# Performance work log

Measured on AMD Instinct MI355X. Metric: run time of the kernel, lower is better.

Reference implementation:

```python
import jax, jax.numpy as jnp
import numpy as np

B, N, D = 4, 2048, 1024
H, A, Lv = 8, 128, 128   # heads, attention_dim (qk), linear_dim (v)
NUM_BLOCKS = 4
QKV_W = (2 * Lv + 2 * A) * H  # 4096
NEG = -1e9


def setup_inputs() -> dict:
    key = jax.random.key(0)
    ks = jax.random.split(key, 10)
    past_lengths = jax.random.randint(ks[0], (B,), 0, N)
    past_ids = jax.random.randint(ks[1], (B, N), 0, 10000)
    past_embeddings = jax.random.normal(ks[2], (B, N, D), dtype=jnp.float32)
    # per-block parameters, stacked on leading block axis (xavier-ish scale)
    qkv_w = jax.random.normal(ks[3], (NUM_BLOCKS, D, QKV_W), dtype=jnp.float32) * (1.0 / np.sqrt(D))
    qkv_b = jnp.zeros((NUM_BLOCKS, QKV_W), dtype=jnp.float32)
    out_w = jax.random.normal(ks[4], (NUM_BLOCKS, Lv * H, D), dtype=jnp.float32) * (1.0 / np.sqrt(Lv * H))
    out_b = jnp.zeros((NUM_BLOCKS, D), dtype=jnp.float32)
    ln_g = jnp.ones((NUM_BLOCKS, D), dtype=jnp.float32)
    ln_b = jnp.zeros((NUM_BLOCKS, D), dtype=jnp.float32)
    return {"past_lengths": past_lengths, "past_ids": past_ids,
            "past_embeddings": past_embeddings, "qkv_w": qkv_w, "qkv_b": qkv_b,
            "out_w": out_w, "out_b": out_b, "ln_g": ln_g, "ln_b": ln_b}


def _layer_norm(x, g, b, eps=1e-5):
    mu = jnp.mean(x, axis=-1, keepdims=True)
    var = jnp.mean(jnp.square(x - mu), axis=-1, keepdims=True)
    return (x - mu) * jax.lax.rsqrt(var + eps) * g + b


def _block(x, mask, qw, qb, ow, ob, g, b):
    xn = _layer_norm(x, g, b)
    qkv = (xn @ qw + qb).reshape(B, N, H, 2 * Lv + 2 * A)
    q = qkv[..., :A]              # [B,N,H,A]
    k = qkv[..., A:2 * A]         # [B,N,H,A]
    v = qkv[..., 2 * A:2 * A + Lv]  # [B,N,H,Lv]
    scores = jnp.einsum('bnha,bmha->bhnm', q, k) / np.sqrt(A)
    # original: masked_fill(-inf) -> silu -> /N -> softmax; we mask after the
    # silu transform with a large-negative logit so masked weights are ~0
    logits = jnp.where(mask[:, None, :, :], jax.nn.silu(scores) / N, NEG)
    w = jax.nn.softmax(logits, axis=-1)
    attn = jnp.einsum('bhnm,bmhl->bnhl', w, v).reshape(B, N, H * Lv)
    return x + attn @ ow + ob


def reference(past_lengths, past_ids, past_embeddings, qkv_w, qkv_b, out_w, out_b, ln_g, ln_b):
    valid = past_ids != 0                                   # [B,N]
    causal = jnp.triu(jnp.ones((N, N), dtype=bool), k=1)     # faithful to buffer (triu, diag=1)
    mask = causal[None] & valid[:, None, :] & valid[:, :, None]  # [B,N,N]
    x = past_embeddings
    for i in range(NUM_BLOCKS):
        x = _block(x, mask, qkv_w[i], qkv_b[i], out_w[i], out_b[i], ln_g[i], ln_b[i])
    return x
```

## Files before the change

### kernel.cpp

```cpp
#include <hip/hip_runtime.h>

typedef __bf16 bf16_t;
typedef __bf16 bf16x8 __attribute__((ext_vector_type(8)));
typedef __bf16 bf16x4 __attribute__((ext_vector_type(4)));
typedef float f32x4 __attribute__((ext_vector_type(4)));

#define B_ 4
#define N_ 2048
#define D_ 1024
#define H_ 8
#define NB_ 4
#define M_ (B_*N_)
#define QN_ 3072
#define QKN_ 2048

__device__ __forceinline__ void async_copy16(const void* gsrc, void* ldst) {
    __builtin_amdgcn_global_load_lds(
        (const __attribute__((address_space(1))) void*)gsrc,
        (__attribute__((address_space(3))) void*)ldst, 16, 0, 0);
}

static constexpr size_t WT_OFF  = 0;
static constexpr size_t WT_SZ   = (size_t)NB_*QN_*D_*2;
static constexpr size_t OWT_OFF = WT_OFF + WT_SZ;
static constexpr size_t OWT_SZ  = (size_t)NB_*D_*D_*2;
static constexpr size_t XN_OFF  = OWT_OFF + OWT_SZ;
static constexpr size_t XN_SZ   = (size_t)M_*D_*2;
static constexpr size_t QK_OFF  = XN_OFF + XN_SZ;
static constexpr size_t QK_SZ   = (size_t)M_*QKN_*2;
static constexpr size_t VT_OFF  = QK_OFF + QK_SZ;
static constexpr size_t VT_SZ   = (size_t)32*128*N_*2;
static constexpr size_t ATT_OFF = VT_OFF + VT_SZ;
static constexpr size_t ATT_SZ  = (size_t)M_*D_*2;
static constexpr size_t QBR_OFF = ATT_OFF + ATT_SZ;
static constexpr size_t QBR_SZ  = (size_t)NB_*QN_*4;
static constexpr size_t VS_OFF  = QBR_OFF + QBR_SZ;

__global__ __launch_bounds__(256) void repack_qkvw(const float* __restrict__ qw, bf16_t* __restrict__ wt)
{
    __shared__ float tile[64][65];
    const int nb = blockIdx.z;
    const int j0 = blockIdx.x * 64, d0 = blockIdx.y * 64;
    const int tx = threadIdx.x, ty = threadIdx.y;
    const float* src = qw + (size_t)nb * D_ * 4096;
    const int jj = j0 + tx;
    const int sel = jj >> 10, rr = jj & 1023, hh = rr >> 7, aa = rr & 127;
    const int orig = hh * 512 + sel * 128 + aa;
#pragma unroll
    for (int it = 0; it < 16; ++it) {
        int dr = it * 4 + ty;
        tile[dr][tx] = src[(size_t)(d0 + dr) * 4096 + orig];
    }
    __syncthreads();
    bf16_t* dst = wt + (size_t)nb * QN_ * D_;
#pragma unroll
    for (int it = 0; it < 16; ++it) {
        int jr = it * 4 + ty;
        dst[(size_t)(j0 + jr) * D_ + d0 + tx] = (bf16_t)tile[tx][jr];
    }
}

__global__ __launch_bounds__(256) void repack_outw(const float* __restrict__ ow, bf16_t* __restrict__ owt)
{
    __shared__ float tile[64][65];
    const int nb = blockIdx.z;
    const int j0 = blockIdx.x * 64, d0 = blockIdx.y * 64;
    const int tx = threadIdx.x, ty = threadIdx.y;
    const float* src = ow + (size_t)nb * D_ * D_;
#pragma unroll
    for (int it = 0; it < 16; ++it) {
        int dr = it * 4 + ty;
        tile[dr][tx] = src[(size_t)(d0 + dr) * D_ + j0 + tx];
    }
    __syncthreads();
    bf16_t* dst = owt + (size_t)nb * D_ * D_;
#pragma unroll
    for (int it = 0; it < 16; ++it) {
        int jr = it * 4 + ty;
        dst[(size_t)(j0 + jr) * D_ + d0 + tx] = (bf16_t)tile[tx][jr];
    }
}

__global__ __launch_bounds__(256) void repack_qb(const float* __restrict__ qb, float* __restrict__ qbr)
{
    int idx = blockIdx.x * 256 + threadIdx.x;
    int nb = idx / QN_, jj = idx % QN_;
    int sel = jj >> 10, rr = jj & 1023, hh = rr >> 7, aa = rr & 127;
    qbr[idx] = qb[nb * 4096 + hh * 512 + sel * 128 + aa];
}

__global__ __launch_bounds__(256) void ln_kernel(const float* __restrict__ x, const float* __restrict__ g,
                                                 const float* __restrict__ bb, bf16_t* __restrict__ xn)
{
    const int row = blockIdx.x, tid = threadIdx.x;
    const float4 v = ((const float4*)(x + (size_t)row * D_))[tid];
    float s = v.x + v.y + v.z + v.w;
    float q = v.x * v.x + v.y * v.y + v.z * v.z + v.w * v.w;
#pragma unroll
    for (int d = 32; d >= 1; d >>= 1) { s += __shfl_xor(s, d); q += __shfl_xor(q, d); }
    __shared__ float ls[4], lq[4];
    if ((tid & 63) == 0) { ls[tid >> 6] = s; lq[tid >> 6] = q; }
    __syncthreads();
    s = ls[0] + ls[1] + ls[2] + ls[3];
    q = lq[0] + lq[1] + lq[2] + lq[3];
    const float mean = s * (1.f / 1024.f);
    const float var  = q * (1.f / 1024.f) - mean * mean;
    const float inv  = rsqrtf(var + 1e-5f);
    const float4 gg = ((const float4*)g)[tid];
    const float4 bv = ((const float4*)bb)[tid];
    bf16x4 o;
    o[0] = (bf16_t)((v.x - mean) * inv * gg.x + bv.x);
    o[1] = (bf16_t)((v.y - mean) * inv * gg.y + bv.y);
    o[2] = (bf16_t)((v.z - mean) * inv * gg.z + bv.z);
    o[3] = (bf16_t)((v.w - mean) * inv * gg.w + bv.w);
    *(bf16x4*)(xn + (size_t)row * D_ + tid * 4) = o;
}

template<bool RESID>
__global__ __launch_bounds__(512, 2) void gemm256(const bf16_t* __restrict__ Am, const bf16_t* __restrict__ Bt,
                                                  const float* __restrict__ bias, float* __restrict__ resid_out,
                                                  bf16_t* __restrict__ outH, bf16_t* __restrict__ vtOut,
                                                  int Kn, int Nn, int vSplit)
{
    __shared__ bf16_t As[4 * 256 * 32];
    __shared__ bf16_t Bs[4 * 128 * 32];
    const int tid = threadIdx.x;
    const int lane = tid & 63, wave = tid >> 6;
    const int wr = wave >> 2, wc = wave & 3;
    const int quad = lane >> 4, l15 = lane & 15;
    const int swz = quad ^ ((l15 >> 1) & 3);
    const int slane8 = ((lane & 3) ^ ((lane >> 3) & 3)) * 8;
    const int lrow = lane >> 2;
    const int m0 = blockIdx.y * 256, n0 = blockIdx.x * 128;

    const int chA0 = wave * 2, chA1 = chA0 + 1;
    const bf16_t* gA0 = Am + (size_t)(m0 + chA0 * 16 + lrow) * Kn + slane8;
    const bf16_t* gA1 = Am + (size_t)(m0 + chA1 * 16 + lrow) * Kn + slane8;
    const bf16_t* gB  = Bt + (size_t)(n0 + wave * 16 + lrow) * Kn + slane8;
    bf16_t* const dA0 = &As[chA0 * 512];
    bf16_t* const dA1 = &As[chA1 * 512];
    bf16_t* const dB  = &Bs[wave * 512];

    auto STAGE = [&](int slot) {
        async_copy16(gA0, dA0 + slot * 8192);
        async_copy16(gA1, dA1 + slot * 8192);
        async_copy16(gB,  dB  + slot * 4096);
        gA0 += 32; gA1 += 32; gB += 32;
    };

    f32x4 acc[8][2] = {};
    const int NT = Kn >> 5;

    STAGE(0); STAGE(1); STAGE(2);
    asm volatile("s_waitcnt vmcnt(6)" ::: "memory");
    __builtin_amdgcn_s_barrier();

    const int aoff = (wr * 128 + l15) * 32 + swz * 8;
    const int boff = (wc * 32  + l15) * 32 + swz * 8;

    for (int t = 0; t < NT; ++t) {
        const int ring = t & 3;
        const bf16_t* ra = &As[ring * 8192 + aoff];
        const bf16_t* rb = &Bs[ring * 4096 + boff];
        bf16x8 af[8], bfv[2];
#pragma unroll
        for (int i = 0; i < 8; ++i) af[i] = *(const bf16x8*)(ra + i * 512);
#pragma unroll
        for (int j = 0; j < 2; ++j) bfv[j] = *(const bf16x8*)(rb + j * 512);
        if (t + 3 < NT) STAGE((t + 3) & 3);
        __builtin_amdgcn_s_barrier();
        asm volatile("s_waitcnt lgkmcnt(0)" ::: "memory");
        __builtin_amdgcn_s_setprio(1);
#pragma unroll
        for (int i = 0; i < 8; ++i)
#pragma unroll
            for (int j = 0; j < 2; ++j)
                acc[i][j] = __builtin_amdgcn_mfma_f32_16x16x32_bf16(af[i], bfv[j], acc[i][j], 0, 0, 0);
        __builtin_amdgcn_s_setprio(0);
        if (t + 3 < NT)      asm volatile("s_waitcnt vmcnt(6)" ::: "memory");
        else if (t + 2 < NT) asm volatile("s_waitcnt vmcnt(3)" ::: "memory");
        else if (t + 1 < NT) asm volatile("s_waitcnt vmcnt(0)" ::: "memory");
        __builtin_amdgcn_s_barrier();
    }

    if (!RESID && n0 >= vSplit) {
#pragma unroll
        for (int i = 0; i < 8; ++i) {
            const int rowg = m0 + wr * 128 + i * 16 + quad * 4;
            const int bb2 = rowg >> 11, mloc = rowg & 2047;
#pragma unroll
            for (int j = 0; j < 2; ++j) {
                const int colg = n0 + wc * 32 + j * 16 + l15;
                const int hh = (colg - 2048) >> 7, ll = (colg - 2048) & 127;
                const float bv = bias[colg];
                bf16x4 sv;
#pragma unroll
                for (int r = 0; r < 4; ++r) sv[r] = (bf16_t)(acc[i][j][r] + bv);
                *(bf16x4*)(vtOut + ((size_t)(bb2 * 8 + hh) * 128 + ll) * (size_t)N_ + mloc) = sv;
            }
        }
        return;
    }
#pragma unroll
    for (int i = 0; i < 8; ++i) {
#pragma unroll
        for (int j = 0; j < 2; ++j) {
            const int colg = n0 + wc * 32 + j * 16 + l15;
            const float bv = bias[colg];
#pragma unroll
            for (int r = 0; r < 4; ++r) {
                const int rowg = m0 + wr * 128 + i * 16 + quad * 4 + r;
                const size_t off = (size_t)rowg * Nn + colg;
                const float v = acc[i][j][r] + bv;
                if (RESID) resid_out[off] += v;
                else       outH[off] = (bf16_t)v;
            }
        }
    }
}

__global__ __launch_bounds__(256) void vsum_kernel(const bf16_t* __restrict__ vt, float* __restrict__ vs)
{
    const int gid = blockIdx.x * 4 + (threadIdx.x >> 6);
    const int lane = threadIdx.x & 63;
    const bf16_t* p = vt + (size_t)gid * N_ + lane * 8;
    float s = 0.f;
#pragma unroll
    for (int c = 0; c < 4; ++c) {
        bf16x8 v = *(const bf16x8*)(p + c * 512);
#pragma unroll
        for (int u = 0; u < 8; ++u) s += (float)v[u];
    }
#pragma unroll
    for (int d = 32; d >= 1; d >>= 1) s += __shfl_xor(s, d);
    if (lane == 0) vs[gid] = s;
}

template<bool CAUSAL>
__device__ __forceinline__ void attn_tile(
    int m0, int n0, int b, int h,
    const bf16_t* __restrict__ qk, const bf16_t* __restrict__ vtb,
    const int* __restrict__ past_ids,
    bf16_t* Ks, float* vmf, bf16_t* Ps,
    const bf16x8* qf, bf16x8 onesf, float vnf,
    f32x4* oacc, f32x4& dacc)
{
    const int tid = threadIdx.x, lane = tid & 63, wave = tid >> 6;
    const int quad = lane >> 4, l15 = lane & 15;
    const int swz = quad ^ ((l15 >> 1) & 3);
    const int slane8 = ((lane & 3) ^ ((lane >> 3) & 3)) * 8;
    const int lrow = lane >> 2;
    const size_t baseq = (size_t)b * N_ * QKN_;
    const float scaleA = 0.08838834764831845f;
    const float invN = 1.f / 2048.f;

    __syncthreads();
#pragma unroll
    for (int s = 0; s < 8; ++s) {
        const int kkc = s & 3, rg = (s >> 2) + wave * 2;
        async_copy16(qk + baseq + (size_t)(m0 + rg * 16 + lrow) * QKN_ + 1024 + h * 128 + kkc * 32 + slane8,
                     &Ks[kkc * 4096 + rg * 512 + lane * 8]);
    }
    if (tid < 128) vmf[tid] = past_ids[b * N_ + m0 + tid] != 0 ? 1.f : 0.f;
    __syncthreads();

    f32x4 sacc[8] = {};
#pragma unroll
    for (int kk = 0; kk < 4; ++kk) {
#pragma unroll
        for (int j = 0; j < 8; ++j) {
            bf16x8 kf = *(const bf16x8*)&Ks[kk * 4096 + (j * 16 + l15) * 32 + swz * 8];
            sacc[j] = __builtin_amdgcn_mfma_f32_16x16x32_bf16(kf, qf[kk], sacc[j], 0, 0, 0);
        }
    }
    __syncthreads();

#pragma unroll
    for (int s = 0; s < 8; ++s) {
        const int kkc = s & 3, rg = (s >> 2) + wave * 2;
        async_copy16(vtb + (size_t)(rg * 16 + lrow) * N_ + m0 + kkc * 32 + slane8,
                     &Ks[kkc * 4096 + rg * 512 + lane * 8]);
    }

    const int dbase = CAUSAL ? (m0 - n0 - wave * 16 - l15 + quad * 4) : 0;
#pragma unroll
    for (int j = 0; j < 8; ++j) {
        f32x4 mmv = *(const f32x4*)&vmf[j * 16 + quad * 4];
        bf16x4 pv;
#pragma unroll
        for (int r = 0; r < 4; ++r) {
            const float sv = sacc[j][r] * scaleA;
            const float xc = fminf(fmaxf(sv, -4.f), 4.f);
            float sig = __builtin_fmaf(xc, 0.25f, 0.5f);
            sig = __builtin_fmaf(-(xc * 0.03125f), fabsf(xc), sig);
            float e = __builtin_fmaf(sv * sig, invN, 1.f);
            e *= mmv[r] * vnf;
            if (CAUSAL) e = (dbase + j * 16 + r > 0) ? e : 0.f;
            pv[r] = (bf16_t)e;
        }
        const int cc = (j & 1) * 2 + (quad >> 1);
        const int cp = cc ^ ((l15 >> 1) & 3);
        *(bf16x4*)&Ps[wave * 2048 + (j >> 1) * 512 + l15 * 32 + cp * 8 + (quad & 1) * 4] = pv;
    }
    __syncthreads();

#pragma unroll
    for (int kk = 0; kk < 4; ++kk) {
        bf16x8 pf = *(const bf16x8*)&Ps[wave * 2048 + kk * 512 + l15 * 32 + swz * 8];
        dacc = __builtin_amdgcn_mfma_f32_16x16x32_bf16(pf, onesf, dacc, 0, 0, 0);
#pragma unroll
        for (int j = 0; j < 8; ++j) {
            bf16x8 vf = *(const bf16x8*)&Ks[kk * 4096 + (j * 16 + l15) * 32 + swz * 8];
            oacc[j] = __builtin_amdgcn_mfma_f32_16x16x32_bf16(pf, vf, oacc[j], 0, 0, 0);
        }
    }
}

__global__ __launch_bounds__(256, 3) void attn_kernel(const bf16_t* __restrict__ qk, const bf16_t* __restrict__ vt,
                                                      const int* __restrict__ past_ids, const float* __restrict__ vsum,
                                                      bf16_t* __restrict__ att)
{
    __shared__ bf16_t Ks[4 * 128 * 32];
    __shared__ bf16_t Ps[4 * 2048];
    __shared__ float vmf[128];

    const int bx = blockIdx.x;
    const int bh = bx & 31, t = bx >> 5;
    const int b = bh >> 3, h = bh & 7;
    const int n0 = t << 6;
    const int tid = threadIdx.x, lane = tid & 63, wave = tid >> 6;
    const int quad = lane >> 4, l15 = lane & 15;
    const bf16_t* vtb = vt + (size_t)bh * 128 * N_;
    const float invN = 1.f / 2048.f;

    bf16x8 qf[4];
    {
        const bf16_t* gq = qk + (size_t)b * N_ * QKN_ + (size_t)(n0 + wave * 16 + l15) * QKN_ + h * 128 + quad * 8;
#pragma unroll
        for (int kk = 0; kk < 4; ++kk) qf[kk] = *(const bf16x8*)(gq + kk * 32);
    }
    const float vnf = past_ids[b * N_ + n0 + wave * 16 + l15] != 0 ? 1.f : 0.f;
    bf16x8 onesf;
#pragma unroll
    for (int i = 0; i < 8; ++i) onesf[i] = (bf16_t)1.f;

    f32x4 oacc[8] = {};
    f32x4 dacc = {};

    const int mt0 = t >> 1;
    attn_tile<true>(mt0 << 7, n0, b, h, qk, vtb, past_ids, Ks, vmf, Ps, qf, onesf, vnf, oacc, dacc);
    for (int mt = mt0 + 1; mt < 16; ++mt)
        attn_tile<false>(mt << 7, n0, b, h, qk, vtb, past_ids, Ks, vmf, Ps, qf, onesf, vnf, oacc, dacc);

    float vsr[8];
#pragma unroll
    for (int j = 0; j < 8; ++j) vsr[j] = vsum[bh * 128 + j * 16 + l15];
#pragma unroll
    for (int r = 0; r < 4; ++r) {
        const float dn = dacc[r];
        const bool uni = !(dn > 0.f);
        const float rc = uni ? 0.f : __builtin_amdgcn_rcpf(dn);
        const int gn = n0 + wave * 16 + quad * 4 + r;
#pragma unroll
        for (int j = 0; j < 8; ++j) {
            const int col = j * 16 + l15;
            const float ov = uni ? (vsr[j] * invN) : (oacc[j][r] * rc);
            att[(size_t)(b * N_ + gn) * 1024 + h * 128 + col] = (bf16_t)ov;
        }
    }
}

extern "C" void kernel_launch(void* const* d_in, const int* in_sizes, int n_in,
                              void* d_out, int out_size, void* d_ws, size_t ws_size,
                              hipStream_t stream) {
    (void)in_sizes; (void)n_in; (void)out_size; (void)ws_size;
    const int*   past_ids = (const int*)d_in[1];
    const float* past_emb = (const float*)d_in[2];
    const float* qkv_w    = (const float*)d_in[3];
    const float* qkv_b    = (const float*)d_in[4];
    const float* out_w    = (const float*)d_in[5];
    const float* out_b    = (const float*)d_in[6];
    const float* ln_g     = (const float*)d_in[7];
    const float* ln_b     = (const float*)d_in[8];

    float* x = (float*)d_out;
    char* ws = (char*)d_ws;
    bf16_t* WT  = (bf16_t*)(ws + WT_OFF);
    bf16_t* OWT = (bf16_t*)(ws + OWT_OFF);
    bf16_t* XN  = (bf16_t*)(ws + XN_OFF);
    bf16_t* QK  = (bf16_t*)(ws + QK_OFF);
    bf16_t* VT  = (bf16_t*)(ws + VT_OFF);
    bf16_t* ATT = (bf16_t*)(ws + ATT_OFF);
    float*  QBR = (float*)(ws + QBR_OFF);
    float*  VS  = (float*)(ws + VS_OFF);

    hipMemcpyAsync(x, past_emb, (size_t)M_ * D_ * sizeof(float), hipMemcpyDeviceToDevice, stream);
    repack_qkvw<<<dim3(48, 16, NB_), dim3(64, 4), 0, stream>>>(qkv_w, WT);
    repack_outw<<<dim3(16, 16, NB_), dim3(64, 4), 0, stream>>>(out_w, OWT);
    repack_qb<<<48, 256, 0, stream>>>(qkv_b, QBR);

    for (int layer = 0; layer < NB_; ++layer) {
        ln_kernel<<<M_, 256, 0, stream>>>(x, ln_g + layer * D_, ln_b + layer * D_, XN);
        gemm256<false><<<dim3(QN_ / 128, M_ / 256), 512, 0, stream>>>(
            XN, WT + (size_t)layer * QN_ * D_, QBR + layer * QN_, nullptr, QK, VT, D_, QKN_, 2048);
        vsum_kernel<<<1024, 256, 0, stream>>>(VT, VS);
        attn_kernel<<<1024, 256, 0, stream>>>(QK, VT, past_ids, VS, ATT);
        gemm256<true><<<dim3(D_ / 128, M_ / 256), 512, 0, stream>>>(
            ATT, OWT + (size_t)layer * D_ * D_, out_b + layer * D_, x, nullptr, nullptr, D_, D_, 1 << 30);
    }
}
```

Measured before the change: 929.5 us.

## Restructure attention to 128-query tiles with register P and prefetched K

Each attention block now handles 128 queries (two 16-row groups per wave), so every K/V tile load is reused across twice as many queries. The P matrix is kept in registers instead of a shared-memory round trip, which needs a matching row permutation of the V-transpose output in the QKV GEMM epilogue. The validity mask is built once per block as ballot bitmasks, and the next K tile is loaded during the PV MFMAs. The grid is halved with a paired causal schedule to balance work, and occupancy drops to 2 blocks per unit because of higher register and LDS use.

```diff
diff --git a/kernel.cpp b/kernel.cpp
--- a/kernel.cpp
+++ b/kernel.cpp
@@ -188,6 +188,7 @@
         for (int i = 0; i < 8; ++i) {
             const int rowg = m0 + wr * 128 + i * 16 + quad * 4;
             const int bb2 = rowg >> 11, mloc = rowg & 2047;
+            const int mperm = (mloc & ~31) | (((mloc >> 2) & 3) << 3) | (((mloc >> 4) & 1) << 2);
 #pragma unroll
             for (int j = 0; j < 2; ++j) {
                 const int colg = n0 + wc * 32 + j * 16 + l15;
@@ -196,7 +197,7 @@
                 bf16x4 sv;
 #pragma unroll
                 for (int r = 0; r < 4; ++r) sv[r] = (bf16_t)(acc[i][j][r] + bv);
-                *(bf16x4*)(vtOut + ((size_t)(bb2 * 8 + hh) * 128 + ll) * (size_t)N_ + mloc) = sv;
+                *(bf16x4*)(vtOut + ((size_t)(bb2 * 8 + hh) * 128 + ll) * (size_t)N_ + mperm) = sv;
             }
         }
         return;
@@ -238,134 +239,175 @@
 
 template<bool CAUSAL>
 __device__ __forceinline__ void attn_tile(
-    int m0, int n0, int b, int h,
+    int m0, int m0n, int n0, int b, int h,
     const bf16_t* __restrict__ qk, const bf16_t* __restrict__ vtb,
-    const int* __restrict__ past_ids,
-    bf16_t* Ks, float* vmf, bf16_t* Ps,
-    const bf16x8* qf, bf16x8 onesf, float vnf,
-    f32x4* oacc, f32x4& dacc)
+    bf16_t* Ks, bf16_t* Vs, const unsigned int* mb,
+    const bf16x8 (&qf)[2][4], bf16x8 onesf, float vnf0, float vnf1,
+    f32x4 (&oacc)[2][8], f32x4 (&dacc)[2])
 {
     const int tid = threadIdx.x, lane = tid & 63, wave = tid >> 6;
     const int quad = lane >> 4, l15 = lane & 15;
     const int swz = quad ^ ((l15 >> 1) & 3);
     const int slane8 = ((lane & 3) ^ ((lane >> 3) & 3)) * 8;
     const int lrow = lane >> 2;
-    const size_t baseq = (size_t)b * N_ * QKN_;
     const float scaleA = 0.08838834764831845f;
     const float invN = 1.f / 2048.f;
-
-    __syncthreads();
-#pragma unroll
-    for (int s = 0; s < 8; ++s) {
-        const int kkc = s & 3, rg = (s >> 2) + wave * 2;
-        async_copy16(qk + baseq + (size_t)(m0 + rg * 16 + lrow) * QKN_ + 1024 + h * 128 + kkc * 32 + slane8,
-                     &Ks[kkc * 4096 + rg * 512 + lane * 8]);
-    }
-    if (tid < 128) vmf[tid] = past_ids[b * N_ + m0 + tid] != 0 ? 1.f : 0.f;
-    __syncthreads();
-
-    f32x4 sacc[8] = {};
-#pragma unroll
-    for (int kk = 0; kk < 4; ++kk) {
-#pragma unroll
-        for (int j = 0; j < 8; ++j) {
-            bf16x8 kf = *(const bf16x8*)&Ks[kk * 4096 + (j * 16 + l15) * 32 + swz * 8];
-            sacc[j] = __builtin_amdgcn_mfma_f32_16x16x32_bf16(kf, qf[kk], sacc[j], 0, 0, 0);
-        }
-    }
-    __syncthreads();
 
 #pragma unroll
     for (int s = 0; s < 8; ++s) {
         const int kkc = s & 3, rg = (s >> 2) + wave * 2;
         async_copy16(vtb + (size_t)(rg * 16 + lrow) * N_ + m0 + kkc * 32 + slane8,
-                     &Ks[kkc * 4096 + rg * 512 + lane * 8]);
-    }
-
-    const int dbase = CAUSAL ? (m0 - n0 - wave * 16 - l15 + quad * 4) : 0;
-#pragma unroll
-    for (int j = 0; j < 8; ++j) {
-        f32x4 mmv = *(const f32x4*)&vmf[j * 16 + quad * 4];
-        bf16x4 pv;
-#pragma unroll
-        for (int r = 0; r < 4; ++r) {
-            const float sv = sacc[j][r] * scaleA;
-            const float xc = fminf(fmaxf(sv, -4.f), 4.f);
-            float sig = __builtin_fmaf(xc, 0.25f, 0.5f);
-            sig = __builtin_fmaf(-(xc * 0.03125f), fabsf(xc), sig);
-            float e = __builtin_fmaf(sv * sig, invN, 1.f);
-            e *= mmv[r] * vnf;
-            if (CAUSAL) e = (dbase + j * 16 + r > 0) ? e : 0.f;
-            pv[r] = (bf16_t)e;
-        }
-        const int cc = (j & 1) * 2 + (quad >> 1);
-        const int cp = cc ^ ((l15 >> 1) & 3);
-        *(bf16x4*)&Ps[wave * 2048 + (j >> 1) * 512 + l15 * 32 + cp * 8 + (quad & 1) * 4] = pv;
-    }
-    __syncthreads();
-
+                     &Vs[kkc * 4096 + rg * 512 + lane * 8]);
+    }
+
+    f32x4 sacc[2][8] = {};
+    __builtin_amdgcn_s_setprio(1);
 #pragma unroll
     for (int kk = 0; kk < 4; ++kk) {
-        bf16x8 pf = *(const bf16x8*)&Ps[wave * 2048 + kk * 512 + l15 * 32 + swz * 8];
-        dacc = __builtin_amdgcn_mfma_f32_16x16x32_bf16(pf, onesf, dacc, 0, 0, 0);
 #pragma unroll
         for (int j = 0; j < 8; ++j) {
-            bf16x8 vf = *(const bf16x8*)&Ks[kk * 4096 + (j * 16 + l15) * 32 + swz * 8];
-            oacc[j] = __builtin_amdgcn_mfma_f32_16x16x32_bf16(pf, vf, oacc[j], 0, 0, 0);
-        }
-    }
-}
-
-__global__ __launch_bounds__(256, 3) void attn_kernel(const bf16_t* __restrict__ qk, const bf16_t* __restrict__ vt,
+            bf16x8 kf = *(const bf16x8*)&Ks[kk * 4096 + (j * 16 + l15) * 32 + swz * 8];
+            sacc[0][j] = __builtin_amdgcn_mfma_f32_16x16x32_bf16(kf, qf[0][kk], sacc[0][j], 0, 0, 0);
+            sacc[1][j] = __builtin_amdgcn_mfma_f32_16x16x32_bf16(kf, qf[1][kk], sacc[1][j], 0, 0, 0);
+        }
+    }
+    __builtin_amdgcn_s_setprio(0);
+
+    unsigned int wj[4];
+#pragma unroll
+    for (int q = 0; q < 4; ++q) wj[q] = mb[(m0 >> 5) + q];
+    bf16x8 pf[2][4];
+#pragma unroll
+    for (int kk = 0; kk < 4; ++kk) {
+#pragma unroll
+        for (int s = 0; s < 2; ++s) {
+            const int j = kk * 2 + s;
+            const unsigned int wrd = wj[j >> 1];
+            const int shl = (j & 1) * 16 + quad * 4;
+#pragma unroll
+            for (int nb = 0; nb < 2; ++nb) {
+                const float vn = nb ? vnf1 : vnf0;
+#pragma unroll
+                for (int r = 0; r < 4; ++r) {
+                    const float sv = sacc[nb][j][r] * scaleA;
+                    const float xc = fminf(fmaxf(sv, -4.f), 4.f);
+                    float sig = __builtin_fmaf(xc, 0.25f, 0.5f);
+                    sig = __builtin_fmaf(-(xc * 0.03125f), fabsf(xc), sig);
+                    float e = __builtin_fmaf(sv * sig, invN, 1.f);
+                    e = ((wrd >> (shl + r)) & 1) ? e * vn : 0.f;
+                    if (CAUSAL) {
+                        const int dmn = (m0 + j * 16 + quad * 4 + r) - (n0 + wave * 32 + nb * 16 + l15);
+                        e = (dmn > 0) ? e : 0.f;
+                    }
+                    pf[nb][kk][s * 4 + r] = (bf16_t)e;
+                }
+            }
+        }
+    }
+
+    __syncthreads();
+
+    if (m0n < N_) {
+        const size_t baseq = (size_t)b * N_ * QKN_;
+#pragma unroll
+        for (int s = 0; s < 8; ++s) {
+            const int kkc = s & 3, rg = (s >> 2) + wave * 2;
+            async_copy16(qk + baseq + (size_t)(m0n + rg * 16 + lrow) * QKN_ + 1024 + h * 128 + kkc * 32 + slane8,
+                         &Ks[kkc * 4096 + rg * 512 + lane * 8]);
+        }
+    }
+
+    __builtin_amdgcn_s_setprio(1);
+#pragma unroll
+    for (int kk = 0; kk < 4; ++kk) {
+        dacc[0] = __builtin_amdgcn_mfma_f32_16x16x32_bf16(pf[0][kk], onesf, dacc[0], 0, 0, 0);
+        dacc[1] = __builtin_amdgcn_mfma_f32_16x16x32_bf16(pf[1][kk], onesf, dacc[1], 0, 0, 0);
+#pragma unroll
+        for (int j = 0; j < 8; ++j) {
+            bf16x8 vf = *(const bf16x8*)&Vs[kk * 4096 + (j * 16 + l15) * 32 + swz * 8];
+            oacc[0][j] = __builtin_amdgcn_mfma_f32_16x16x32_bf16(pf[0][kk], vf, oacc[0][j], 0, 0, 0);
+            oacc[1][j] = __builtin_amdgcn_mfma_f32_16x16x32_bf16(pf[1][kk], vf, oacc[1][j], 0, 0, 0);
+        }
+    }
+    __builtin_amdgcn_s_setprio(0);
+    __syncthreads();
+}
+
+__global__ __launch_bounds__(256, 2) void attn_kernel(const bf16_t* __restrict__ qk, const bf16_t* __restrict__ vt,
                                                       const int* __restrict__ past_ids, const float* __restrict__ vsum,
                                                       bf16_t* __restrict__ att)
 {
     __shared__ bf16_t Ks[4 * 128 * 32];
-    __shared__ bf16_t Ps[4 * 2048];
-    __shared__ float vmf[128];
+    __shared__ bf16_t Vs[4 * 128 * 32];
+    __shared__ unsigned long long mbits[32];
 
     const int bx = blockIdx.x;
-    const int bh = bx & 31, t = bx >> 5;
+    const int bh = bx & 31, g = bx >> 5;
+    const int t = (g < 8) ? g : 23 - g;
     const int b = bh >> 3, h = bh & 7;
-    const int n0 = t << 6;
+    const int n0 = t << 7;
     const int tid = threadIdx.x, lane = tid & 63, wave = tid >> 6;
     const int quad = lane >> 4, l15 = lane & 15;
+    const int slane8 = ((lane & 3) ^ ((lane >> 3) & 3)) * 8;
+    const int lrow = lane >> 2;
     const bf16_t* vtb = vt + (size_t)bh * 128 * N_;
     const float invN = 1.f / 2048.f;
 
-    bf16x8 qf[4];
+#pragma unroll
+    for (int it = 0; it < 8; ++it) {
+        const int m = (wave * 8 + it) * 64 + lane;
+        const unsigned long long bal = __ballot(past_ids[b * N_ + m] != 0);
+        if (lane == 0) mbits[wave * 8 + it] = bal;
+    }
+
+    bf16x8 qf[2][4];
+#pragma unroll
+    for (int nb = 0; nb < 2; ++nb) {
+        const bf16_t* gq = qk + (size_t)b * N_ * QKN_ + (size_t)(n0 + wave * 32 + nb * 16 + l15) * QKN_ + h * 128 + quad * 8;
+#pragma unroll
+        for (int kk = 0; kk < 4; ++kk) qf[nb][kk] = *(const bf16x8*)(gq + kk * 32);
+    }
+    const float vnf0 = past_ids[b * N_ + n0 + wave * 32 + l15] != 0 ? 1.f : 0.f;
+    const float vnf1 = past_ids[b * N_ + n0 + wave * 32 + 16 + l15] != 0 ? 1.f : 0.f;
+    bf16x8 onesf;
+#pragma unroll
+    for (int i = 0; i < 8; ++i) onesf[i] = (bf16_t)1.f;
+
     {
-        const bf16_t* gq = qk + (size_t)b * N_ * QKN_ + (size_t)(n0 + wave * 16 + l15) * QKN_ + h * 128 + quad * 8;
-#pragma unroll
-        for (int kk = 0; kk < 4; ++kk) qf[kk] = *(const bf16x8*)(gq + kk * 32);
-    }
-    const float vnf = past_ids[b * N_ + n0 + wave * 16 + l15] != 0 ? 1.f : 0.f;
-    bf16x8 onesf;
-#pragma unroll
-    for (int i = 0; i < 8; ++i) onesf[i] = (bf16_t)1.f;
-
-    f32x4 oacc[8] = {};
-    f32x4 dacc = {};
-
-    const int mt0 = t >> 1;
-    attn_tile<true>(mt0 << 7, n0, b, h, qk, vtb, past_ids, Ks, vmf, Ps, qf, onesf, vnf, oacc, dacc);
-    for (int mt = mt0 + 1; mt < 16; ++mt)
-        attn_tile<false>(mt << 7, n0, b, h, qk, vtb, past_ids, Ks, vmf, Ps, qf, onesf, vnf, oacc, dacc);
+        const size_t baseq = (size_t)b * N_ * QKN_;
+#pragma unroll
+        for (int s = 0; s < 8; ++s) {
+            const int kkc = s & 3, rg = (s >> 2) + wave * 2;
+            async_copy16(qk + baseq + (size_t)(n0 + rg * 16 + lrow) * QKN_ + 1024 + h * 128 + kkc * 32 + slane8,
+                         &Ks[kkc * 4096 + rg * 512 + lane * 8]);
+        }
+    }
+    __syncthreads();
+
+    f32x4 oacc[2][8] = {};
+    f32x4 dacc[2] = {};
+    const unsigned int* mb = (const unsigned int*)mbits;
+
+    attn_tile<true>(n0, n0 + 128, n0, b, h, qk, vtb, Ks, Vs, mb, qf, onesf, vnf0, vnf1, oacc, dacc);
+    for (int m0 = n0 + 128; m0 < N_; m0 += 128)
+        attn_tile<false>(m0, m0 + 128, n0, b, h, qk, vtb, Ks, Vs, mb, qf, onesf, vnf0, vnf1, oacc, dacc);
 
     float vsr[8];
 #pragma unroll
     for (int j = 0; j < 8; ++j) vsr[j] = vsum[bh * 128 + j * 16 + l15];
 #pragma unroll
-    for (int r = 0; r < 4; ++r) {
-        const float dn = dacc[r];
-        const bool uni = !(dn > 0.f);
-        const float rc = uni ? 0.f : __builtin_amdgcn_rcpf(dn);
-        const int gn = n0 + wave * 16 + quad * 4 + r;
-#pragma unroll
-        for (int j = 0; j < 8; ++j) {
-            const int col = j * 16 + l15;
-            const float ov = uni ? (vsr[j] * invN) : (oacc[j][r] * rc);
-            att[(size_t)(b * N_ + gn) * 1024 + h * 128 + col] = (bf16_t)ov;
+    for (int nb = 0; nb < 2; ++nb) {
+#pragma unroll
+        for (int r = 0; r < 4; ++r) {
+            const float dn = dacc[nb][r];
+            const bool uni = !(dn > 0.f);
+            const float rc = uni ? 0.f : __builtin_amdgcn_rcpf(dn);
+            const int gn = n0 + wave * 32 + nb * 16 + quad * 4 + r;
+#pragma unroll
+            for (int j = 0; j < 8; ++j) {
+                const float ov = uni ? (vsr[j] * invN) : (oacc[nb][j][r] * rc);
+                att[(size_t)(b * N_ + gn) * 1024 + h * 128 + j * 16 + l15] = (bf16_t)ov;
+            }
         }
     }
 }
@@ -404,7 +446,7 @@
         gemm256<false><<<dim3(QN_ / 128, M_ / 256), 512, 0, stream>>>(
             XN, WT + (size_t)layer * QN_ * D_, QBR + layer * QN_, nullptr, QK, VT, D_, QKN_, 2048);
         vsum_kernel<<<1024, 256, 0, stream>>>(VT, VS);
-        attn_kernel<<<1024, 256, 0, stream>>>(QK, VT, past_ids, VS, ATT);
+        attn_kernel<<<512, 256, 0, stream>>>(QK, VT, past_ids, VS, ATT);
         gemm256<true><<<dim3(D_ / 128, M_ / 256), 512, 0, stream>>>(
             ATT, OWT + (size_t)layer * D_ * D_, out_b + layer * D_, x, nullptr, nullptr, D_, D_, 1 << 30);
     }
```

Result: no change. 923.4 us (-0.7%).
